# Kernel tuning notes

Hardware: AMD Instinct MI355X
Metric: run time of the kernel (lower is better)

The kernel has to match this reference:

```python
import jax, jax.numpy as jnp
import numpy as np

B, C, N, K, H = 8, 32, 4096, 32, 4  # batch, d_model, num_points, knn, heads
D = C // H
LN_EPS = 1e-5
ATT_EPS = 1e-6


def setup_inputs() -> dict:
    key = jax.random.key(0)
    ks = jax.random.split(key, 12)
    s = 0.05
    return {
        "search_feat": jax.random.normal(ks[0], (B, C, N), jnp.float32),
        "search_xyz": jax.random.normal(ks[1], (B, N, 3), jnp.float32),
        # pos MLP: Linear(3,32)+ReLU+Linear(32,32), weights stored [in,out]
        "w_pos1": jax.random.normal(ks[2], (3, 32), jnp.float32) * s,
        "b_pos1": jnp.zeros((32,), jnp.float32),
        "w_pos2": jax.random.normal(ks[3], (32, 32), jnp.float32) * s,
        "b_pos2": jnp.zeros((32,), jnp.float32),
        "w_q": jax.random.normal(ks[4], (C, C), jnp.float32) * s,
        "w_k": jax.random.normal(ks[5], (C, C), jnp.float32) * s,
        "w_v": jax.random.normal(ks[6], (C, C), jnp.float32) * s,
        "w_merge": jax.random.normal(ks[7], (C, C), jnp.float32) * s,
        "ln1_g": jnp.ones((C,), jnp.float32),
        "ln1_b": jnp.zeros((C,), jnp.float32),
        "w_mlp1": jax.random.normal(ks[8], (2 * C, 2 * C), jnp.float32) * s,
        "w_mlp2": jax.random.normal(ks[9], (2 * C, C), jnp.float32) * s,
        "ln2_g": jnp.ones((C,), jnp.float32),
        "ln2_b": jnp.zeros((C,), jnp.float32),
    }


def _layernorm(x, g, b):
    m = jnp.mean(x, axis=-1, keepdims=True)
    v = jnp.mean((x - m) ** 2, axis=-1, keepdims=True)
    return g * (x - m) * jax.lax.rsqrt(v + LN_EPS) + b


def _elu1(x):
    return jax.nn.elu(x) + 1.0


def reference(search_feat, search_xyz, w_pos1, b_pos1, w_pos2, b_pos2,
              w_q, w_k, w_v, w_merge, ln1_g, ln1_b, w_mlp1, w_mlp2,
              ln2_g, ln2_b):
    b, c, n = search_feat.shape
    h, d, k = H, C // H, K

    xt = jnp.transpose(search_feat, (0, 2, 1))  # [B,N,C]
    # knn in feature space: pd = -||xi||^2 + 2 xi.xj - ||xj||^2 (neg sq dist)
    xx = jnp.sum(xt * xt, axis=-1)  # [B,N]
    pd = 2.0 * jnp.einsum('bnc,bmc->bnm', xt, xt) - xx[:, :, None] - xx[:, None, :]
    idx = jax.lax.top_k(pd, k)[1]  # [B,N,K] nearest (incl. self)

    gather = jax.vmap(lambda f, i: f[i])  # per-batch gather
    fea_knn = gather(xt, idx)            # [B,N,K,C]
    xyz_knn = gather(search_xyz, idx)    # [B,N,K,3]

    def pos_mlp(z):
        return jax.nn.relu(z @ w_pos1 + b_pos1) @ w_pos2 + b_pos2

    q_in = xt + pos_mlp(search_xyz)      # [B,N,C]  (query, L=1)
    kv_in = fea_knn + pos_mlp(xyz_knn)   # [B,N,K,C]

    Q = (q_in @ w_q).reshape(b, n, h, d)          # [B,N,H,D]
    Ky = (kv_in @ w_k).reshape(b, n, k, h, d)     # [B,N,K,H,D]
    V = (kv_in @ w_v).reshape(b, n, k, h, d)

    Qf = _elu1(Q)
    Kf = _elu1(Ky)
    Vn = V / k  # v_length = K
    KV = jnp.einsum('bnkhd,bnkhv->bnhdv', Kf, Vn)
    Z = 1.0 / (jnp.einsum('bnhd,bnhd->bnh', Qf, Kf.sum(axis=2)) + ATT_EPS)
    msg = jnp.einsum('bnhd,bnhdv,bnh->bnhv', Qf, KV, Z) * k  # [B,N,H,D]

    msg = msg.reshape(b, n, c) @ w_merge
    msg = _layernorm(msg, ln1_g, ln1_b)
    msg = jnp.concatenate([xt, msg], axis=-1)          # [B,N,2C]
    msg = jax.nn.relu(msg @ w_mlp1) @ w_mlp2           # [B,N,C]
    msg = _layernorm(msg, ln2_g, ln2_b)
    return jnp.transpose(xt + msg, (0, 2, 1))          # [B,C,N]
```

## Files before the change

kernel.cpp:

```cpp
#include <hip/hip_runtime.h>
#include <math.h>

#define BB 8
#define CC 32
#define NN 4096
#define KNN 32
#define NP (BB*NN)

#define OFF_XT  0u
#define OFF_QF  1048576u
#define OFF_KV  2097152u
#define OFF_XX  4194304u
#define OFF_IDX 4227072u
#define OFF_XH  5275648u
#define OFF_XL  5799936u
#define OFF_MSG 5275648u

typedef _Float16 f16x8 __attribute__((ext_vector_type(8)));
typedef float f32x4 __attribute__((ext_vector_type(4)));
#define MFMA16(A,B,C) __builtin_amdgcn_mfma_f32_16x16x32_f16(A,B,C,0,0,0)

__device__ __forceinline__ float elu1(float x) {
    return x > 0.f ? x + 1.f : expf(x);
}

__global__ __launch_bounds__(256) void k_transpose(const float* __restrict__ feat,
                                                   float* __restrict__ xt,
                                                   _Float16* __restrict__ Xh,
                                                   _Float16* __restrict__ Xl,
                                                   float* __restrict__ xx) {
    __shared__ float tile[32][65];
    int b = blockIdx.y;
    int n0 = blockIdx.x * 64;
    int t = threadIdx.x;
    int nn = t & 63, cr = t >> 6;
#pragma unroll
    for (int r = 0; r < 8; ++r) {
        int c = r * 4 + cr;
        tile[c][nn] = feat[((size_t)b * 32 + c) * NN + n0 + nn];
    }
    __syncthreads();
    int c2 = t & 31, nr = t >> 5;
#pragma unroll
    for (int r = 0; r < 8; ++r) {
        int nl = r * 8 + nr;
        size_t gi = ((size_t)b * NN + n0 + nl) * 32 + c2;
        float v = tile[c2][nl];
        xt[gi] = v;
        _Float16 hv = (_Float16)v;
        Xh[gi] = hv;
        Xl[gi] = (_Float16)(v - (float)hv);
    }
    if (t < 64) {
        float s = 0.f;
#pragma unroll
        for (int c = 0; c < 32; ++c) { float u = tile[c][t]; s += u * u; }
        xx[(size_t)b * NN + n0 + t] = s;
    }
}

__global__ __launch_bounds__(256, 2) void k_prep(
        const float* __restrict__ xt, const float* __restrict__ xyz,
        const float* __restrict__ w_pos1, const float* __restrict__ b_pos1,
        const float* __restrict__ w_pos2, const float* __restrict__ b_pos2,
        const float* __restrict__ w_q, const float* __restrict__ w_k,
        const float* __restrict__ w_v,
        float* __restrict__ Qf, float* __restrict__ KV) {
    __shared__ float sW2[1024], sWq[1024], sWk[1024], sWv[1024];
    int t = threadIdx.x;
    for (int i = t; i < 1024; i += 256) {
        sW2[i] = w_pos2[i];
        sWq[i] = w_q[i];
        sWk[i] = w_k[i];
        sWv[i] = w_v[i];
    }
    int lane = t & 31;
    int g = t >> 5;
    float w1c0 = w_pos1[lane], w1c1 = w_pos1[32 + lane], w1c2 = w_pos1[64 + lane];
    float b1c = b_pos1[lane], b2c = b_pos2[lane];
    __syncthreads();
#pragma unroll 1
    for (int p = blockIdx.x * 8 + g; p < NP; p += gridDim.x * 8) {
        asm volatile("" ::: "memory");
        float x0 = xyz[(size_t)p * 3 + 0];
        float x1 = xyz[(size_t)p * 3 + 1];
        float x2 = xyz[(size_t)p * 3 + 2];
        float h = fmaxf(x0 * w1c0 + x1 * w1c1 + x2 * w1c2 + b1c, 0.f);
        float P = b2c;
#pragma unroll 8
        for (int j = 0; j < 32; ++j) P += __shfl(h, j, 32) * sW2[j * 32 + lane];
        float xv = xt[(size_t)p * 32 + lane];
        float qin = xv + P;
        float qa = 0.f, ka = 0.f, va = 0.f;
#pragma unroll 8
        for (int j = 0; j < 32; ++j) {
            float qj = __shfl(qin, j, 32);
            qa += qj * sWq[j * 32 + lane];
            ka += qj * sWk[j * 32 + lane];
            va += qj * sWv[j * 32 + lane];
        }
        Qf[(size_t)p * 32 + lane] = elu1(qa);
        float2 kvv;
        kvv.x = elu1(ka);
        kvv.y = va;
        *(((float2*)(KV + (size_t)p * 64)) + lane) = kvv;
    }
}

__global__ __launch_bounds__(256, 2) void k_knn(
        const _Float16* __restrict__ Xh, const _Float16* __restrict__ Xl,
        const float* __restrict__ xt, const float* __restrict__ xx,
        unsigned* __restrict__ idxg) {
    __shared__ unsigned histU[32 * 132];
    __shared__ unsigned outIdx[32][32];
    __shared__ unsigned tieIdx[32][96];
    __shared__ int sT[32];
    __shared__ unsigned sBase[32];
    __shared__ float sFloor[32];
    __shared__ unsigned outCnt[32], tieCnt[32];
    __shared__ float sM2;
    __shared__ float redbuf[4];

    int bid = blockIdx.x;
    int b = bid & 7;
    int n0 = (bid >> 3) << 5;
    int t = threadIdx.x;
    int lane = t & 63, wv = t >> 6;
    size_t bbase = (size_t)b * NN;

    for (int i = t; i < 32 * 132; i += 256) histU[i] = 0u;
    if (t < 32) { outCnt[t] = 0u; tieCnt[t] = 0u; }

    float lm = 0.f;
    for (int i = t; i < NN; i += 256) lm = fmaxf(lm, xx[bbase + i]);
#pragma unroll
    for (int off = 32; off >= 1; off >>= 1) lm = fmaxf(lm, __shfl_xor(lm, off, 64));
    if (lane == 0) redbuf[wv] = lm;
    __syncthreads();
    if (t == 0) sM2 = fmaxf(fmaxf(redbuf[0], redbuf[1]), fmaxf(redbuf[2], redbuf[3]));
    __syncthreads();
    float M2 = sM2;

    int al = lane & 15;
    int kgrp = lane >> 4;
    int ak = kgrp * 8;
    const _Float16* Xhb = Xh + bbase * 32;
    const _Float16* Xlb = Xl + bbase * 32;
    const float* xxb = xx + bbase;
    f16x8 Ah0 = *(const f16x8*)(Xhb + (size_t)(n0 + al) * 32 + ak);
    f16x8 Al0 = *(const f16x8*)(Xlb + (size_t)(n0 + al) * 32 + ak);
    f16x8 Ah1 = *(const f16x8*)(Xhb + (size_t)(n0 + 16 + al) * 32 + ak);
    f16x8 Al1 = *(const f16x8*)(Xlb + (size_t)(n0 + 16 + al) * 32 + ak);

    const float C127 = 127.99f;
    float sc2[8], scn[8], c0a[8];
    unsigned rowW[8];
    int rowloc8[8];
#pragma unroll
    for (int r = 0; r < 8; ++r) {
        int rowloc = (r < 4 ? 0 : 16) + kgrp * 4 + (r & 3);
        float xxi = xxb[n0 + rowloc];
        float scale = C127 / (2.f * (xxi + M2));
        sc2[r] = scale + scale;
        scn[r] = -scale;
        c0a[r] = __builtin_fmaf(-xxi, scale, C127);
        rowW[r] = (unsigned)rowloc * 132u;
        rowloc8[r] = rowloc;
    }

    unsigned cp0 = (unsigned)(wv * 1024 + al);
    unsigned akB = (unsigned)ak * 2u;
    const char* XhbB = (const char*)Xhb;
    const char* XlbB = (const char*)Xlb;

#pragma unroll 1
    for (int tt = 0; tt < 8; ++tt) {
        unsigned cp = cp0 + (unsigned)(tt << 4);
        f16x8 Bh = *(const f16x8*)(XhbB + cp * 64u + akB);
        f16x8 Bl = *(const f16x8*)(XlbB + cp * 64u + akB);
        float xxj = xxb[cp];
        f32x4 z = {0.f, 0.f, 0.f, 0.f};
        f32x4 u0 = MFMA16(Al0, Bl, z); u0 = MFMA16(Ah0, Bl, u0);
        f32x4 w0 = MFMA16(Al0, Bh, z); w0 = MFMA16(Ah0, Bh, w0);
        f32x4 u1 = MFMA16(Al1, Bl, z); u1 = MFMA16(Ah1, Bl, u1);
        f32x4 w1 = MFMA16(Al1, Bh, z); w1 = MFMA16(Ah1, Bh, w1);
#pragma unroll
        for (int r = 0; r < 8; ++r) {
            float a = (r < 4) ? (u0[r] + w0[r]) : (u1[r - 4] + w1[r - 4]);
            float bcol = __builtin_fmaf(xxj, scn[r], c0a[r]);
            float qf = __builtin_fmaf(a, sc2[r], bcol);
            float qc = __builtin_amdgcn_fmed3f(qf, 0.f, C127);
            atomicAdd(&histU[rowW[r] + (unsigned)qc], 1u);
        }
    }
    __syncthreads();

#pragma unroll 1
    for (int rr = 0; rr < 8; ++rr) {
        int row = wv * 8 + rr;
        const unsigned* Hr = histU + row * 132;
        unsigned cl = Hr[2 * lane], ch = Hr[2 * lane + 1];
        unsigned ss = cl + ch;
        unsigned acc = ss;
#pragma unroll
        for (int off = 1; off < 64; off <<= 1) {
            unsigned vv = __shfl_down(acc, off, 64);
            if (lane + off < 64) acc += vv;
        }
        unsigned run = acc - ss;
        int Tl = -1;
        if (run < 32u && run + ch >= 32u) Tl = 2 * lane + 1;
        run += ch;
        if (Tl < 0 && run < 32u && run + cl >= 32u) Tl = 2 * lane;
        unsigned long long bal = __ballot(Tl >= 0);
        int src = __ffsll(bal) - 1;
        int Tv = __shfl(Tl, src, 64);
        if (lane == 0) sFloor[row] = (Tv <= 0) ? -3.0e38f : (float)Tv;
    }
    __syncthreads();

    float fb1[8];
#pragma unroll
    for (int r = 0; r < 8; ++r) fb1[r] = sFloor[rowloc8[r]];

    {
        unsigned cpc = cp0 + (8u << 4);
        f16x8 Bh_c = *(const f16x8*)(XhbB + cpc * 64u + akB);
        f16x8 Bl_c = *(const f16x8*)(XlbB + cpc * 64u + akB);
        float xxj_c = xxb[cpc];
#pragma unroll 1
        for (int tt = 8; tt < 64; ++tt) {
            int tn = (tt + 1 < 64) ? (tt + 1) : 8;
            unsigned cpn = cp0 + (unsigned)(tn << 4);
            f16x8 Bh_n = *(const f16x8*)(XhbB + cpn * 64u + akB);
            f16x8 Bl_n = *(const f16x8*)(XlbB + cpn * 64u + akB);
            float xxj_n = xxb[cpn];
            f32x4 z = {0.f, 0.f, 0.f, 0.f};
            f32x4 u0 = MFMA16(Al0, Bl_c, z); u0 = MFMA16(Ah0, Bl_c, u0);
            f32x4 w0 = MFMA16(Al0, Bh_c, z); w0 = MFMA16(Ah0, Bh_c, w0);
            f32x4 u1 = MFMA16(Al1, Bl_c, z); u1 = MFMA16(Ah1, Bl_c, u1);
            f32x4 w1 = MFMA16(Al1, Bh_c, z); w1 = MFMA16(Ah1, Bh_c, w1);
            float bcol[8];
#pragma unroll
            for (int r = 0; r < 8; ++r) bcol[r] = __builtin_fmaf(xxj_c, scn[r], c0a[r]);
#pragma unroll
            for (int r = 0; r < 8; ++r) {
                float a = (r < 4) ? (u0[r] + w0[r]) : (u1[r - 4] + w1[r - 4]);
                float qf = __builtin_fmaf(a, sc2[r], bcol[r]);
                if (qf >= fb1[r]) {
                    float qc = __builtin_amdgcn_fmed3f(qf, 0.f, C127);
                    atomicAdd(&histU[rowW[r] + (unsigned)qc], 1u);
                }
            }
            Bh_c = Bh_n; Bl_c = Bl_n; xxj_c = xxj_n;
        }
    }
    __syncthreads();

#pragma unroll 1
    for (int rr = 0; rr < 8; ++rr) {
        int row = wv * 8 + rr;
        const unsigned* Hr = histU + row * 132;
        unsigned cl = Hr[2 * lane], ch = Hr[2 * lane + 1];
        unsigned ss = cl + ch;
        unsigned acc = ss;
#pragma unroll
        for (int off = 1; off < 64; off <<= 1) {
            unsigned vv = __shfl_down(acc, off, 64);
            if (lane + off < 64) acc += vv;
        }
        unsigned run = acc - ss;
        int Tl = -1; unsigned bl = 0;
        if (run < 32u && run + ch >= 32u) { Tl = 2 * lane + 1; bl = run; }
        run += ch;
        if (Tl < 0 && run < 32u && run + cl >= 32u) { Tl = 2 * lane; bl = run; }
        unsigned long long bal = __ballot(Tl >= 0);
        int src = __ffsll(bal) - 1;
        int Tv = __shfl(Tl, src, 64);
        unsigned bv = (unsigned)__shfl((int)bl, src, 64);
        if (lane == 0) { sT[row] = Tv; sBase[row] = bv; }
    }
    __syncthreads();

    float Tin[8], Tlo[8];
#pragma unroll
    for (int r = 0; r < 8; ++r) {
        int T = sT[rowloc8[r]];
        Tin[r] = (float)(T + 1);
        Tlo[r] = (T == 0) ? -3.0e38f : (float)T;
    }

    {
        f16x8 Bh_c = *(const f16x8*)(XhbB + cp0 * 64u + akB);
        f16x8 Bl_c = *(const f16x8*)(XlbB + cp0 * 64u + akB);
        float xxj_c = xxb[cp0];
#pragma unroll 1
        for (int tt = 0; tt < 64; ++tt) {
            unsigned cp = cp0 + (unsigned)(tt << 4);
            unsigned cpn = cp0 + (unsigned)(((tt + 1) & 63) << 4);
            f16x8 Bh_n = *(const f16x8*)(XhbB + cpn * 64u + akB);
            f16x8 Bl_n = *(const f16x8*)(XlbB + cpn * 64u + akB);
            float xxj_n = xxb[cpn];
            f32x4 z = {0.f, 0.f, 0.f, 0.f};
            f32x4 u0 = MFMA16(Al0, Bl_c, z); u0 = MFMA16(Ah0, Bl_c, u0);
            f32x4 w0 = MFMA16(Al0, Bh_c, z); w0 = MFMA16(Ah0, Bh_c, w0);
            f32x4 u1 = MFMA16(Al1, Bl_c, z); u1 = MFMA16(Ah1, Bl_c, u1);
            f32x4 w1 = MFMA16(Al1, Bh_c, z); w1 = MFMA16(Ah1, Bh_c, w1);
            float bcol[8];
#pragma unroll
            for (int r = 0; r < 8; ++r) bcol[r] = __builtin_fmaf(xxj_c, scn[r], c0a[r]);
#pragma unroll
            for (int r = 0; r < 8; ++r) {
                float a = (r < 4) ? (u0[r] + w0[r]) : (u1[r - 4] + w1[r - 4]);
                float qf = __builtin_fmaf(a, sc2[r], bcol[r]);
                if (qf >= Tlo[r]) {
                    unsigned row = rowW[r] / 132u;
                    if (qf >= Tin[r]) {
                        unsigned pos = atomicAdd(&outCnt[row], 1u);
                        outIdx[row][pos] = cp;
                    } else {
                        unsigned tp = atomicAdd(&tieCnt[row], 1u);
                        if (tp < 96u) tieIdx[row][tp] = cp;
                    }
                }
            }
            Bh_c = Bh_n; Bl_c = Bl_n; xxj_c = xxj_n;
        }
    }
    __syncthreads();

#pragma unroll 1
    for (int rr = 0; rr < 8; ++rr) {
        int row = wv * 8 + rr;
        int gr = n0 + row;
        unsigned bA = sBase[row];
        int need = 32 - (int)bA;
        if (need <= 0) continue;
        int nt = (int)tieCnt[row]; if (nt > 96) nt = 96;
        const float* xr = xt + (bbase + gr) * 32;
        float xxi_r = xxb[gr];
        float v0 = -INFINITY, v1 = -INFINITY;
        int i0 = 0x7fffffff, i1 = 0x7fffffff;
        bool a0v = lane < nt, a1v = lane + 64 < nt;
        if (a0v) {
            int c = (int)tieIdx[row][lane];
            const float* xc = xt + (bbase + c) * 32;
            float dot = 0.f;
#pragma unroll
            for (int ch = 0; ch < 32; ch += 4) {
                float4 rv = *(const float4*)(xr + ch);
                float4 cv = *(const float4*)(xc + ch);
                dot = __builtin_fmaf(rv.x, cv.x, dot);
                dot = __builtin_fmaf(rv.y, cv.y, dot);
                dot = __builtin_fmaf(rv.z, cv.z, dot);
                dot = __builtin_fmaf(rv.w, cv.w, dot);
            }
            v0 = 2.f * dot - xxi_r - xxb[c];
            i0 = c;
        }
        if (a1v) {
            int c = (int)tieIdx[row][lane + 64];
            const float* xc = xt + (bbase + c) * 32;
            float dot = 0.f;
#pragma unroll
            for (int ch = 0; ch < 32; ch += 4) {
                float4 rv = *(const float4*)(xr + ch);
                float4 cv = *(const float4*)(xc + ch);
                dot = __builtin_fmaf(rv.x, cv.x, dot);
                dot = __builtin_fmaf(rv.y, cv.y, dot);
                dot = __builtin_fmaf(rv.z, cv.z, dot);
                dot = __builtin_fmaf(rv.w, cv.w, dot);
            }
            v1 = 2.f * dot - xxi_r - xxb[c];
            i1 = c;
        }
        for (int it = 0; it < need; ++it) {
            float bvv = -INFINITY; int bj2 = 0x7fffffff;
            if (a0v && (v0 > bvv || (v0 == bvv && i0 < bj2))) { bvv = v0; bj2 = i0; }
            if (a1v && (v1 > bvv || (v1 == bvv && i1 < bj2))) { bvv = v1; bj2 = i1; }
#pragma unroll
            for (int off = 1; off < 64; off <<= 1) {
                float ov = __shfl_xor(bvv, off, 64);
                int oj = __shfl_xor(bj2, off, 64);
                if (ov > bvv || (ov == bvv && oj < bj2)) { bvv = ov; bj2 = oj; }
            }
            if (a0v && i0 == bj2) a0v = false;
            if (a1v && i1 == bj2) a1v = false;
            if (lane == 0) outIdx[row][bA + it] = (unsigned)bj2;
        }
    }
    __syncthreads();

    for (int i = t; i < 1024; i += 256)
        idxg[(bbase + n0 + (i >> 5)) * 32 + (i & 31)] = outIdx[i >> 5][i & 31];
}

__global__ __launch_bounds__(256) void k_attn(
        const float* __restrict__ Qf, const float* __restrict__ KV,
        const unsigned* __restrict__ idxg, float* __restrict__ msg) {
    int t = threadIdx.x;
    int wv = t >> 6, lane = t & 63;
    int l32 = lane & 31;
    int bid = blockIdx.x;
    int b = bid & 7;
    int p = b * NN + (bid >> 3) * 8 + wv * 2 + (lane >> 5);
    size_t bbase = (size_t)b * NN;
    const char* KVb = (const char*)(KV + bbase * 64);
    float q = Qf[(size_t)p * 32 + l32];
    int jv = (int)idxg[(size_t)p * 32 + l32];
    unsigned laneoff = (unsigned)l32 * 8u;
    float zacc = 0.f, macc = 0.f;
#pragma unroll 8
    for (int k = 0; k < 32; ++k) {
        int j = __shfl(jv, k, 32);
        unsigned off = ((unsigned)j << 8) + laneoff;
        float2 kv = *(const float2*)(KVb + off);
        float s = q * kv.x;
        s += __shfl_xor(s, 1, 8);
        s += __shfl_xor(s, 2, 8);
        s += __shfl_xor(s, 4, 8);
        zacc += s;
        macc = __builtin_fmaf(s, kv.y, macc);
    }
    float Z = 1.f / (zacc + 1e-6f);
    msg[(size_t)p * 32 + l32] = macc * Z;
}

__global__ __launch_bounds__(256, 2) void k_post(
        const float* __restrict__ msg, const float* __restrict__ xt,
        const float* __restrict__ w_merge,
        const float* __restrict__ ln1_g, const float* __restrict__ ln1_b,
        const float* __restrict__ w_mlp1, const float* __restrict__ w_mlp2,
        const float* __restrict__ ln2_g, const float* __restrict__ ln2_b,
        float* __restrict__ out) {
    __shared__ _Float16 wmT[2][32][32];
    __shared__ _Float16 w1T[2][64][64];
    __shared__ _Float16 w2T[2][32][64];
    __shared__ _Float16 sPh[4][16][40], sPl[4][16][40];
    __shared__ _Float16 sHh[4][16][72], sHl[4][16][72];
    int t = threadIdx.x;
    for (int i = t; i < 1024; i += 256) {
        float v = w_merge[i]; int in = i >> 5, o = i & 31;
        _Float16 h = (_Float16)v;
        wmT[0][o][in] = h; wmT[1][o][in] = (_Float16)(v - (float)h);
    }
    for (int i = t; i < 4096; i += 256) {
        float v = w_mlp1[i]; int in = i >> 6, o = i & 63;
        _Float16 h = (_Float16)v;
        w1T[0][o][in] = h; w1T[1][o][in] = (_Float16)(v - (float)h);
    }
    for (int i = t; i < 2048; i += 256) {
        float v = w_mlp2[i]; int in = i >> 5, o = i & 31;
        _Float16 h = (_Float16)v;
        w2T[0][o][in] = h; w2T[1][o][in] = (_Float16)(v - (float)h);
    }
    int wv = t >> 6, lane = t & 63;
    int row = lane & 15, kg = lane >> 4;
    int p0 = blockIdx.x * 64 + wv * 16;
    int b = p0 >> 12;
    float g1a = ln1_g[row], b1a = ln1_b[row], g1b = ln1_g[row + 16], b1b = ln1_b[row + 16];
    float g2a = ln2_g[row], b2a = ln2_b[row], g2b = ln2_g[row + 16], b2b = ln2_b[row + 16];
    __syncthreads();

    f32x4 z4 = {0.f, 0.f, 0.f, 0.f};
    f16x8 Amh, Aml;
    {
        const float* mr = msg + (size_t)(p0 + row) * 32 + kg * 8;
#pragma unroll
        for (int j = 0; j < 8; ++j) {
            float v = mr[j];
            _Float16 h = (_Float16)v;
            Amh[j] = h; Aml[j] = (_Float16)(v - (float)h);
        }
    }
    f32x4 accM[2];
#pragma unroll
    for (int n = 0; n < 2; ++n) {
        f16x8 Bh = *(const f16x8*)&wmT[0][n * 16 + row][kg * 8];
        f16x8 Bl = *(const f16x8*)&wmT[1][n * 16 + row][kg * 8];
        f32x4 a = z4;
        a = MFMA16(Aml, Bl, a); a = MFMA16(Amh, Bl, a);
        a = MFMA16(Aml, Bh, a); a = MFMA16(Amh, Bh, a);
        accM[n] = a;
    }
#pragma unroll
    for (int r = 0; r < 4; ++r) {
        float s0 = accM[0][r], s1 = accM[1][r];
        float sm = s0 + s1;
        sm += __shfl_xor(sm, 1, 64); sm += __shfl_xor(sm, 2, 64);
        sm += __shfl_xor(sm, 4, 64); sm += __shfl_xor(sm, 8, 64);
        float mean = sm * (1.f / 32.f);
        float d0 = s0 - mean, d1 = s1 - mean;
        float vv = d0 * d0 + d1 * d1;
        vv += __shfl_xor(vv, 1, 64); vv += __shfl_xor(vv, 2, 64);
        vv += __shfl_xor(vv, 4, 64); vv += __shfl_xor(vv, 8, 64);
        float rst = rsqrtf(vv * (1.f / 32.f) + 1e-5f);
        float m0 = g1a * d0 * rst + b1a;
        float m1 = g1b * d1 * rst + b1b;
        int pl = kg * 4 + r;
        _Float16 h0 = (_Float16)m0;
        sPh[wv][pl][row] = h0; sPl[wv][pl][row] = (_Float16)(m0 - (float)h0);
        _Float16 h1 = (_Float16)m1;
        sPh[wv][pl][row + 16] = h1; sPl[wv][pl][row + 16] = (_Float16)(m1 - (float)h1);
    }
    __syncthreads();
    f16x8 Axh, Axl;
    {
        const float* xr = xt + (size_t)(p0 + row) * 32 + kg * 8;
#pragma unroll
        for (int j = 0; j < 8; ++j) {
            float v = xr[j];
            _Float16 h = (_Float16)v;
            Axh[j] = h; Axl[j] = (_Float16)(v - (float)h);
        }
    }
    f16x8 Aph = *(const f16x8*)&sPh[wv][row][kg * 8];
    f16x8 Apl = *(const f16x8*)&sPl[wv][row][kg * 8];
    f32x4 accH[4];
#pragma unroll
    for (int n = 0; n < 4; ++n) {
        f16x8 B0h = *(const f16x8*)&w1T[0][n * 16 + row][kg * 8];
        f16x8 B0l = *(const f16x8*)&w1T[1][n * 16 + row][kg * 8];
        f16x8 B1h = *(const f16x8*)&w1T[0][n * 16 + row][32 + kg * 8];
        f16x8 B1l = *(const f16x8*)&w1T[1][n * 16 + row][32 + kg * 8];
        f32x4 a = z4;
        a = MFMA16(Axl, B0l, a); a = MFMA16(Axh, B0l, a);
        a = MFMA16(Axl, B0h, a); a = MFMA16(Axh, B0h, a);
        a = MFMA16(Apl, B1l, a); a = MFMA16(Aph, B1l, a);
        a = MFMA16(Apl, B1h, a); a = MFMA16(Aph, B1h, a);
        accH[n] = a;
    }
#pragma unroll
    for (int n = 0; n < 4; ++n) {
#pragma unroll
        for (int r = 0; r < 4; ++r) {
            float hv = fmaxf(accH[n][r], 0.f);
            int pl = kg * 4 + r;
            _Float16 hh = (_Float16)hv;
            sHh[wv][pl][n * 16 + row] = hh;
            sHl[wv][pl][n * 16 + row] = (_Float16)(hv - (float)hh);
        }
    }
    __syncthreads();
    f16x8 Hh0 = *(const f16x8*)&sHh[wv][row][kg * 8];
    f16x8 Hl0 = *(const f16x8*)&sHl[wv][row][kg * 8];
    f16x8 Hh1 = *(const f16x8*)&sHh[wv][row][32 + kg * 8];
    f16x8 Hl1 = *(const f16x8*)&sHl[wv][row][32 + kg * 8];
    f32x4 accO[2];
#pragma unroll
    for (int n = 0; n < 2; ++n) {
        f16x8 B0h = *(const f16x8*)&w2T[0][n * 16 + row][kg * 8];
        f16x8 B0l = *(const f16x8*)&w2T[1][n * 16 + row][kg * 8];
        f16x8 B1h = *(const f16x8*)&w2T[0][n * 16 + row][32 + kg * 8];
        f16x8 B1l = *(const f16x8*)&w2T[1][n * 16 + row][32 + kg * 8];
        f32x4 a = z4;
        a = MFMA16(Hl0, B0l, a); a = MFMA16(Hh0, B0l, a);
        a = MFMA16(Hl0, B0h, a); a = MFMA16(Hh0, B0h, a);
        a = MFMA16(Hl1, B1l, a); a = MFMA16(Hh1, B1l, a);
        a = MFMA16(Hl1, B1h, a); a = MFMA16(Hh1, B1h, a);
        accO[n] = a;
    }
#pragma unroll
    for (int r = 0; r < 4; ++r) {
        float s0 = accO[0][r], s1 = accO[1][r];
        float sm = s0 + s1;
        sm += __shfl_xor(sm, 1, 64); sm += __shfl_xor(sm, 2, 64);
        sm += __shfl_xor(sm, 4, 64); sm += __shfl_xor(sm, 8, 64);
        float mean = sm * (1.f / 32.f);
        float d0 = s0 - mean, d1 = s1 - mean;
        float vv = d0 * d0 + d1 * d1;
        vv += __shfl_xor(vv, 1, 64); vv += __shfl_xor(vv, 2, 64);
        vv += __shfl_xor(vv, 4, 64); vv += __shfl_xor(vv, 8, 64);
        float rst = rsqrtf(vv * (1.f / 32.f) + 1e-5f);
        float o0 = g2a * d0 * rst + b2a;
        float o1 = g2b * d1 * rst + b2b;
        int pt = p0 + kg * 4 + r;
        int nb = pt & 4095;
        float xv0 = xt[(size_t)pt * 32 + row];
        float xv1 = xt[(size_t)pt * 32 + row + 16];
        out[((size_t)b * 32 + row) * 4096 + nb] = xv0 + o0;
        out[((size_t)b * 32 + row + 16) * 4096 + nb] = xv1 + o1;
    }
}

extern "C" void kernel_launch(void* const* d_in, const int* in_sizes, int n_in,
                              void* d_out, int out_size, void* d_ws, size_t ws_size,
                              hipStream_t stream) {
    const float* feat   = (const float*)d_in[0];
    const float* xyz    = (const float*)d_in[1];
    const float* w_pos1 = (const float*)d_in[2];
    const float* b_pos1 = (const float*)d_in[3];
    const float* w_pos2 = (const float*)d_in[4];
    const float* b_pos2 = (const float*)d_in[5];
    const float* w_q    = (const float*)d_in[6];
    const float* w_k    = (const float*)d_in[7];
    const float* w_v    = (const float*)d_in[8];
    const float* w_mg   = (const float*)d_in[9];
    const float* ln1_g  = (const float*)d_in[10];
    const float* ln1_b  = (const float*)d_in[11];
    const float* w_mlp1 = (const float*)d_in[12];
    const float* w_mlp2 = (const float*)d_in[13];
    const float* ln2_g  = (const float*)d_in[14];
    const float* ln2_b  = (const float*)d_in[15];
    float* ws = (float*)d_ws;
    float* xt = ws + OFF_XT;
    float* Qf = ws + OFF_QF;
    float* KVp = ws + OFF_KV;
    float* xx = ws + OFF_XX;
    unsigned* idxg = (unsigned*)(ws + OFF_IDX);
    _Float16* Xh = (_Float16*)(ws + OFF_XH);
    _Float16* Xl = (_Float16*)(ws + OFF_XL);
    float* msg = ws + OFF_MSG;
    float* out = (float*)d_out;

    k_transpose<<<dim3(64, 8), 256, 0, stream>>>(feat, xt, Xh, Xl, xx);
    k_prep<<<1024, 256, 0, stream>>>(xt, xyz, w_pos1, b_pos1, w_pos2, b_pos2,
                                     w_q, w_k, w_v, Qf, KVp);
    k_knn<<<1024, 256, 0, stream>>>(Xh, Xl, xt, xx, idxg);
    k_attn<<<4096, 256, 0, stream>>>(Qf, KVp, idxg, msg);
    k_post<<<512, 256, 0, stream>>>(msg, xt, w_mg, ln1_g, ln1_b,
                                    w_mlp1, w_mlp2, ln2_g, ln2_b, out);
}
```

Baseline: 246.3 us.

## Use single fp16 split for kNN distance screening with widened tie band

The kNN histogram and candidate passes now compute dot products from a single fp16 copy of the features instead of a hi/lo split, cutting MFMAs per tile from eight to two. The Xl buffer and its writes go away. Quantization now uses one global scale shared by all rows instead of per-row scales. To absorb the coarser precision, the threshold band is widened by ±0.125 buckets, the tie buffer grows to 192 entries, and exact fp32 rescoring handles the extra ties. The first histogram pass also gains a software-prefetched load. The risks are tie-buffer overflow, which would give wrong neighbours, and coarser per-row resolution from the global scale, which makes more candidates land in the tie band.

```diff
diff --git a/kernel.cpp b/kernel.cpp
--- a/kernel.cpp
+++ b/kernel.cpp
@@ -13,7 +13,6 @@
 #define OFF_XX  4194304u
 #define OFF_IDX 4227072u
 #define OFF_XH  5275648u
-#define OFF_XL  5799936u
 #define OFF_MSG 5275648u
 
 typedef _Float16 f16x8 __attribute__((ext_vector_type(8)));
@@ -27,7 +26,6 @@
 __global__ __launch_bounds__(256) void k_transpose(const float* __restrict__ feat,
                                                    float* __restrict__ xt,
                                                    _Float16* __restrict__ Xh,
-                                                   _Float16* __restrict__ Xl,
                                                    float* __restrict__ xx) {
     __shared__ float tile[32][65];
     int b = blockIdx.y;
@@ -47,9 +45,7 @@
         size_t gi = ((size_t)b * NN + n0 + nl) * 32 + c2;
         float v = tile[c2][nl];
         xt[gi] = v;
-        _Float16 hv = (_Float16)v;
-        Xh[gi] = hv;
-        Xl[gi] = (_Float16)(v - (float)hv);
+        Xh[gi] = (_Float16)v;
     }
     if (t < 64) {
         float s = 0.f;
@@ -108,14 +104,13 @@
 }
 
 __global__ __launch_bounds__(256, 2) void k_knn(
-        const _Float16* __restrict__ Xh, const _Float16* __restrict__ Xl,
+        const _Float16* __restrict__ Xh,
         const float* __restrict__ xt, const float* __restrict__ xx,
         unsigned* __restrict__ idxg) {
     __shared__ unsigned histU[32 * 132];
     __shared__ unsigned outIdx[32][32];
-    __shared__ unsigned tieIdx[32][96];
+    __shared__ unsigned tieIdx[32][192];
     __shared__ int sT[32];
-    __shared__ unsigned sBase[32];
     __shared__ float sFloor[32];
     __shared__ unsigned outCnt[32], tieCnt[32];
     __shared__ float sM2;
@@ -139,58 +134,51 @@
     __syncthreads();
     if (t == 0) sM2 = fmaxf(fmaxf(redbuf[0], redbuf[1]), fmaxf(redbuf[2], redbuf[3]));
     __syncthreads();
-    float M2 = sM2;
+    float M = fmaxf(sM2, 1e-20f);
+
+    const float C127 = 127.99f;
+    float s = C127 / (4.f * M);
+    float s2 = s + s;
+    float sneg = -s;
+    float o = 3.f * s * M;
 
     int al = lane & 15;
-    int kgrp = lane >> 4;
-    int ak = kgrp * 8;
+    int kg = lane >> 4;
+    int ak = kg * 8;
     const _Float16* Xhb = Xh + bbase * 32;
-    const _Float16* Xlb = Xl + bbase * 32;
     const float* xxb = xx + bbase;
+
     f16x8 Ah0 = *(const f16x8*)(Xhb + (size_t)(n0 + al) * 32 + ak);
-    f16x8 Al0 = *(const f16x8*)(Xlb + (size_t)(n0 + al) * 32 + ak);
     f16x8 Ah1 = *(const f16x8*)(Xhb + (size_t)(n0 + 16 + al) * 32 + ak);
-    f16x8 Al1 = *(const f16x8*)(Xlb + (size_t)(n0 + 16 + al) * 32 + ak);
-
-    const float C127 = 127.99f;
-    float sc2[8], scn[8], c0a[8];
-    unsigned rowW[8];
-    int rowloc8[8];
-#pragma unroll
-    for (int r = 0; r < 8; ++r) {
-        int rowloc = (r < 4 ? 0 : 16) + kgrp * 4 + (r & 3);
-        float xxi = xxb[n0 + rowloc];
-        float scale = C127 / (2.f * (xxi + M2));
-        sc2[r] = scale + scale;
-        scn[r] = -scale;
-        c0a[r] = __builtin_fmaf(-xxi, scale, C127);
-        rowW[r] = (unsigned)rowloc * 132u;
-        rowloc8[r] = rowloc;
-    }
 
     unsigned cp0 = (unsigned)(wv * 1024 + al);
-    unsigned akB = (unsigned)ak * 2u;
-    const char* XhbB = (const char*)Xhb;
-    const char* XlbB = (const char*)Xlb;
-
+    unsigned rb0 = (unsigned)(kg * 4) * 132u;
+    const f32x4 z = {0.f, 0.f, 0.f, 0.f};
+
+    {
+        f16x8 B_c = *(const f16x8*)(Xhb + (size_t)cp0 * 32 + ak);
+        float xxj_c = xxb[cp0];
 #pragma unroll 1
-    for (int tt = 0; tt < 8; ++tt) {
-        unsigned cp = cp0 + (unsigned)(tt << 4);
-        f16x8 Bh = *(const f16x8*)(XhbB + cp * 64u + akB);
-        f16x8 Bl = *(const f16x8*)(XlbB + cp * 64u + akB);
-        float xxj = xxb[cp];
-        f32x4 z = {0.f, 0.f, 0.f, 0.f};
-        f32x4 u0 = MFMA16(Al0, Bl, z); u0 = MFMA16(Ah0, Bl, u0);
-        f32x4 w0 = MFMA16(Al0, Bh, z); w0 = MFMA16(Ah0, Bh, w0);
-        f32x4 u1 = MFMA16(Al1, Bl, z); u1 = MFMA16(Ah1, Bl, u1);
-        f32x4 w1 = MFMA16(Al1, Bh, z); w1 = MFMA16(Ah1, Bh, w1);
-#pragma unroll
-        for (int r = 0; r < 8; ++r) {
-            float a = (r < 4) ? (u0[r] + w0[r]) : (u1[r - 4] + w1[r - 4]);
-            float bcol = __builtin_fmaf(xxj, scn[r], c0a[r]);
-            float qf = __builtin_fmaf(a, sc2[r], bcol);
-            float qc = __builtin_amdgcn_fmed3f(qf, 0.f, C127);
-            atomicAdd(&histU[rowW[r] + (unsigned)qc], 1u);
+        for (int tt = 0; tt < 8; ++tt) {
+            unsigned cpn = cp0 + (unsigned)((tt + 1) << 4);
+            f16x8 B_n = *(const f16x8*)(Xhb + (size_t)cpn * 32 + ak);
+            float xxj_n = xxb[cpn];
+            f32x4 a0 = MFMA16(Ah0, B_c, z);
+            f32x4 a1 = MFMA16(Ah1, B_c, z);
+            float e = __builtin_fmaf(sneg, xxj_c, o);
+#pragma unroll
+            for (int r = 0; r < 4; ++r) {
+                float qv = __builtin_fmaf(a0[r], s2, e);
+                unsigned bkt = (unsigned)__builtin_amdgcn_fmed3f(qv, 0.f, C127);
+                atomicAdd(&histU[rb0 + (unsigned)(r * 132) + bkt], 1u);
+            }
+#pragma unroll
+            for (int r = 0; r < 4; ++r) {
+                float qv = __builtin_fmaf(a1[r], s2, e);
+                unsigned bkt = (unsigned)__builtin_amdgcn_fmed3f(qv, 0.f, C127);
+                atomicAdd(&histU[rb0 + (unsigned)(2112 + r * 132) + bkt], 1u);
+            }
+            B_c = B_n; xxj_c = xxj_n;
         }
     }
     __syncthreads();
@@ -219,40 +207,43 @@
     }
     __syncthreads();
 
-    float fb1[8];
-#pragma unroll
-    for (int r = 0; r < 8; ++r) fb1[r] = sFloor[rowloc8[r]];
+    float fbA[4], fbB[4];
+#pragma unroll
+    for (int r = 0; r < 4; ++r) {
+        fbA[r] = sFloor[kg * 4 + r];
+        fbB[r] = sFloor[16 + kg * 4 + r];
+    }
 
     {
         unsigned cpc = cp0 + (8u << 4);
-        f16x8 Bh_c = *(const f16x8*)(XhbB + cpc * 64u + akB);
-        f16x8 Bl_c = *(const f16x8*)(XlbB + cpc * 64u + akB);
+        f16x8 B_c = *(const f16x8*)(Xhb + (size_t)cpc * 32 + ak);
         float xxj_c = xxb[cpc];
 #pragma unroll 1
         for (int tt = 8; tt < 64; ++tt) {
             int tn = (tt + 1 < 64) ? (tt + 1) : 8;
             unsigned cpn = cp0 + (unsigned)(tn << 4);
-            f16x8 Bh_n = *(const f16x8*)(XhbB + cpn * 64u + akB);
-            f16x8 Bl_n = *(const f16x8*)(XlbB + cpn * 64u + akB);
+            f16x8 B_n = *(const f16x8*)(Xhb + (size_t)cpn * 32 + ak);
             float xxj_n = xxb[cpn];
-            f32x4 z = {0.f, 0.f, 0.f, 0.f};
-            f32x4 u0 = MFMA16(Al0, Bl_c, z); u0 = MFMA16(Ah0, Bl_c, u0);
-            f32x4 w0 = MFMA16(Al0, Bh_c, z); w0 = MFMA16(Ah0, Bh_c, w0);
-            f32x4 u1 = MFMA16(Al1, Bl_c, z); u1 = MFMA16(Ah1, Bl_c, u1);
-            f32x4 w1 = MFMA16(Al1, Bh_c, z); w1 = MFMA16(Ah1, Bh_c, w1);
-            float bcol[8];
-#pragma unroll
-            for (int r = 0; r < 8; ++r) bcol[r] = __builtin_fmaf(xxj_c, scn[r], c0a[r]);
-#pragma unroll
-            for (int r = 0; r < 8; ++r) {
-                float a = (r < 4) ? (u0[r] + w0[r]) : (u1[r - 4] + w1[r - 4]);
-                float qf = __builtin_fmaf(a, sc2[r], bcol[r]);
-                if (qf >= fb1[r]) {
-                    float qc = __builtin_amdgcn_fmed3f(qf, 0.f, C127);
-                    atomicAdd(&histU[rowW[r] + (unsigned)qc], 1u);
+            f32x4 a0 = MFMA16(Ah0, B_c, z);
+            f32x4 a1 = MFMA16(Ah1, B_c, z);
+            float e = __builtin_fmaf(sneg, xxj_c, o);
+#pragma unroll
+            for (int r = 0; r < 4; ++r) {
+                float qv = __builtin_fmaf(a0[r], s2, e);
+                if (qv >= fbA[r]) {
+                    unsigned bkt = (unsigned)__builtin_amdgcn_fmed3f(qv, 0.f, C127);
+                    atomicAdd(&histU[rb0 + (unsigned)(r * 132) + bkt], 1u);
                 }
             }
-            Bh_c = Bh_n; Bl_c = Bl_n; xxj_c = xxj_n;
+#pragma unroll
+            for (int r = 0; r < 4; ++r) {
+                float qv = __builtin_fmaf(a1[r], s2, e);
+                if (qv >= fbB[r]) {
+                    unsigned bkt = (unsigned)__builtin_amdgcn_fmed3f(qv, 0.f, C127);
+                    atomicAdd(&histU[rb0 + (unsigned)(2112 + r * 132) + bkt], 1u);
+                }
+            }
+            B_c = B_n; xxj_c = xxj_n;
         }
     }
     __syncthreads();
@@ -270,61 +261,69 @@
             if (lane + off < 64) acc += vv;
         }
         unsigned run = acc - ss;
-        int Tl = -1; unsigned bl = 0;
-        if (run < 32u && run + ch >= 32u) { Tl = 2 * lane + 1; bl = run; }
+        int Tl = -1;
+        if (run < 32u && run + ch >= 32u) Tl = 2 * lane + 1;
         run += ch;
-        if (Tl < 0 && run < 32u && run + cl >= 32u) { Tl = 2 * lane; bl = run; }
+        if (Tl < 0 && run < 32u && run + cl >= 32u) Tl = 2 * lane;
         unsigned long long bal = __ballot(Tl >= 0);
         int src = __ffsll(bal) - 1;
         int Tv = __shfl(Tl, src, 64);
-        unsigned bv = (unsigned)__shfl((int)bl, src, 64);
-        if (lane == 0) { sT[row] = Tv; sBase[row] = bv; }
-    }
-    __syncthreads();
-
-    float Tin[8], Tlo[8];
-#pragma unroll
-    for (int r = 0; r < 8; ++r) {
-        int T = sT[rowloc8[r]];
-        Tin[r] = (float)(T + 1);
-        Tlo[r] = (T == 0) ? -3.0e38f : (float)T;
+        if (lane == 0) sT[row] = Tv;
+    }
+    __syncthreads();
+
+    float tinA[4], tloA[4], tinB[4], tloB[4];
+#pragma unroll
+    for (int r = 0; r < 4; ++r) {
+        int TA = sT[kg * 4 + r];
+        int TB = sT[16 + kg * 4 + r];
+        tinA[r] = (float)(TA + 1) + 0.125f;
+        tloA[r] = (float)TA - 0.125f;
+        tinB[r] = (float)(TB + 1) + 0.125f;
+        tloB[r] = (float)TB - 0.125f;
     }
 
     {
-        f16x8 Bh_c = *(const f16x8*)(XhbB + cp0 * 64u + akB);
-        f16x8 Bl_c = *(const f16x8*)(XlbB + cp0 * 64u + akB);
+        f16x8 B_c = *(const f16x8*)(Xhb + (size_t)cp0 * 32 + ak);
         float xxj_c = xxb[cp0];
 #pragma unroll 1
         for (int tt = 0; tt < 64; ++tt) {
             unsigned cp = cp0 + (unsigned)(tt << 4);
             unsigned cpn = cp0 + (unsigned)(((tt + 1) & 63) << 4);
-            f16x8 Bh_n = *(const f16x8*)(XhbB + cpn * 64u + akB);
-            f16x8 Bl_n = *(const f16x8*)(XlbB + cpn * 64u + akB);
+            f16x8 B_n = *(const f16x8*)(Xhb + (size_t)cpn * 32 + ak);
             float xxj_n = xxb[cpn];
-            f32x4 z = {0.f, 0.f, 0.f, 0.f};
-            f32x4 u0 = MFMA16(Al0, Bl_c, z); u0 = MFMA16(Ah0, Bl_c, u0);
-            f32x4 w0 = MFMA16(Al0, Bh_c, z); w0 = MFMA16(Ah0, Bh_c, w0);
-            f32x4 u1 = MFMA16(Al1, Bl_c, z); u1 = MFMA16(Ah1, Bl_c, u1);
-            f32x4 w1 = MFMA16(Al1, Bh_c, z); w1 = MFMA16(Ah1, Bh_c, w1);
-            float bcol[8];
-#pragma unroll
-            for (int r = 0; r < 8; ++r) bcol[r] = __builtin_fmaf(xxj_c, scn[r], c0a[r]);
-#pragma unroll
-            for (int r = 0; r < 8; ++r) {
-                float a = (r < 4) ? (u0[r] + w0[r]) : (u1[r - 4] + w1[r - 4]);
-                float qf = __builtin_fmaf(a, sc2[r], bcol[r]);
-                if (qf >= Tlo[r]) {
-                    unsigned row = rowW[r] / 132u;
-                    if (qf >= Tin[r]) {
-                        unsigned pos = atomicAdd(&outCnt[row], 1u);
-                        outIdx[row][pos] = cp;
+            f32x4 a0 = MFMA16(Ah0, B_c, z);
+            f32x4 a1 = MFMA16(Ah1, B_c, z);
+            float e = __builtin_fmaf(sneg, xxj_c, o);
+#pragma unroll
+            for (int r = 0; r < 4; ++r) {
+                float qv = __builtin_fmaf(a0[r], s2, e);
+                if (qv >= tloA[r]) {
+                    unsigned rl = (unsigned)(kg * 4 + r);
+                    if (qv >= tinA[r]) {
+                        unsigned pos = atomicAdd(&outCnt[rl], 1u);
+                        outIdx[rl][pos] = cp;
                     } else {
-                        unsigned tp = atomicAdd(&tieCnt[row], 1u);
-                        if (tp < 96u) tieIdx[row][tp] = cp;
+                        unsigned tp = atomicAdd(&tieCnt[rl], 1u);
+                        if (tp < 192u) tieIdx[rl][tp] = cp;
                     }
                 }
             }
-            Bh_c = Bh_n; Bl_c = Bl_n; xxj_c = xxj_n;
+#pragma unroll
+            for (int r = 0; r < 4; ++r) {
+                float qv = __builtin_fmaf(a1[r], s2, e);
+                if (qv >= tloB[r]) {
+                    unsigned rl = (unsigned)(16 + kg * 4 + r);
+                    if (qv >= tinB[r]) {
+                        unsigned pos = atomicAdd(&outCnt[rl], 1u);
+                        outIdx[rl][pos] = cp;
+                    } else {
+                        unsigned tp = atomicAdd(&tieCnt[rl], 1u);
+                        if (tp < 192u) tieIdx[rl][tp] = cp;
+                    }
+                }
+            }
+            B_c = B_n; xxj_c = xxj_n;
         }
     }
     __syncthreads();
@@ -333,15 +332,15 @@
     for (int rr = 0; rr < 8; ++rr) {
         int row = wv * 8 + rr;
         int gr = n0 + row;
-        unsigned bA = sBase[row];
+        unsigned bA = outCnt[row];
         int need = 32 - (int)bA;
         if (need <= 0) continue;
-        int nt = (int)tieCnt[row]; if (nt > 96) nt = 96;
+        int nt = (int)tieCnt[row]; if (nt > 192) nt = 192;
         const float* xr = xt + (bbase + gr) * 32;
         float xxi_r = xxb[gr];
-        float v0 = -INFINITY, v1 = -INFINITY;
-        int i0 = 0x7fffffff, i1 = 0x7fffffff;
-        bool a0v = lane < nt, a1v = lane + 64 < nt;
+        float v0 = -INFINITY, v1 = -INFINITY, v2 = -INFINITY;
+        int i0 = 0x7fffffff, i1 = 0x7fffffff, i2 = 0x7fffffff;
+        bool a0v = lane < nt, a1v = lane + 64 < nt, a2v = lane + 128 < nt;
         if (a0v) {
             int c = (int)tieIdx[row][lane];
             const float* xc = xt + (bbase + c) * 32;
@@ -374,10 +373,27 @@
             v1 = 2.f * dot - xxi_r - xxb[c];
             i1 = c;
         }
+        if (a2v) {
+            int c = (int)tieIdx[row][lane + 128];
+            const float* xc = xt + (bbase + c) * 32;
+            float dot = 0.f;
+#pragma unroll
+            for (int ch = 0; ch < 32; ch += 4) {
+                float4 rv = *(const float4*)(xr + ch);
+                float4 cv = *(const float4*)(xc + ch);
+                dot = __builtin_fmaf(rv.x, cv.x, dot);
+                dot = __builtin_fmaf(rv.y, cv.y, dot);
+                dot = __builtin_fmaf(rv.z, cv.z, dot);
+                dot = __builtin_fmaf(rv.w, cv.w, dot);
+            }
+            v2 = 2.f * dot - xxi_r - xxb[c];
+            i2 = c;
+        }
         for (int it = 0; it < need; ++it) {
             float bvv = -INFINITY; int bj2 = 0x7fffffff;
             if (a0v && (v0 > bvv || (v0 == bvv && i0 < bj2))) { bvv = v0; bj2 = i0; }
             if (a1v && (v1 > bvv || (v1 == bvv && i1 < bj2))) { bvv = v1; bj2 = i1; }
+            if (a2v && (v2 > bvv || (v2 == bvv && i2 < bj2))) { bvv = v2; bj2 = i2; }
 #pragma unroll
             for (int off = 1; off < 64; off <<= 1) {
                 float ov = __shfl_xor(bvv, off, 64);
@@ -386,6 +402,7 @@
             }
             if (a0v && i0 == bj2) a0v = false;
             if (a1v && i1 == bj2) a1v = false;
+            if (a2v && i2 == bj2) a2v = false;
             if (lane == 0) outIdx[row][bA + it] = (unsigned)bj2;
         }
     }
@@ -609,14 +626,13 @@
     float* xx = ws + OFF_XX;
     unsigned* idxg = (unsigned*)(ws + OFF_IDX);
     _Float16* Xh = (_Float16*)(ws + OFF_XH);
-    _Float16* Xl = (_Float16*)(ws + OFF_XL);
     float* msg = ws + OFF_MSG;
     float* out = (float*)d_out;
 
-    k_transpose<<<dim3(64, 8), 256, 0, stream>>>(feat, xt, Xh, Xl, xx);
+    k_transpose<<<dim3(64, 8), 256, 0, stream>>>(feat, xt, Xh, xx);
     k_prep<<<1024, 256, 0, stream>>>(xt, xyz, w_pos1, b_pos1, w_pos2, b_pos2,
                                      w_q, w_k, w_v, Qf, KVp);
-    k_knn<<<1024, 256, 0, stream>>>(Xh, Xl, xt, xx, idxg);
+    k_knn<<<1024, 256, 0, stream>>>(Xh, xt, xx, idxg);
     k_attn<<<4096, 256, 0, stream>>>(Qf, KVp, idxg, msg);
     k_post<<<512, 256, 0, stream>>>(msg, xt, w_mg, ln1_g, ln1_b,
                                     w_mlp1, w_mlp2, ln2_g, ln2_b, out);
```

Result: slower. 361.2 us (+46.7%).
